# Kernel optimization log

Hardware: AMD Instinct MI355X
Metric: run time of the kernel (lower is better)

The kernel has to match this reference:

```python
import jax, jax.numpy as jnp
import numpy as np

B, S, D, H = 2, 2048, 1024, 16
HD = D // H  # 64
SCALE = np.sqrt(HD).astype(np.float32)


def setup_inputs() -> dict:
    key = jax.random.key(0)
    k1, k2, k3, k4, k5, k6 = jax.random.split(key, 6)
    hidden_states = jax.random.normal(k1, (B, S, D), dtype=jnp.float32)
    attention_mask = jax.random.randint(k2, (B, 1, S, S), 0, 2) > 0  # bool
    std = 0.02
    W_qkv = jax.random.normal(k3, (D, 3 * D), dtype=jnp.float32) * std
    b_qkv = jnp.zeros((3 * D,), dtype=jnp.float32)
    W_dense = jax.random.normal(k4, (D, D), dtype=jnp.float32) * std
    b_dense = jnp.zeros((D,), dtype=jnp.float32)
    return {
        "hidden_states": hidden_states,
        "attention_mask": attention_mask,
        "W_qkv": W_qkv,
        "b_qkv": b_qkv,
        "W_dense": W_dense,
        "b_dense": b_dense,
    }


def reference(hidden_states, attention_mask, W_qkv, b_qkv, W_dense, b_dense):
    # fused QKV projection: [B,S,3D]
    qkv = hidden_states @ W_qkv + b_qkv
    q, k, v = jnp.split(qkv, 3, axis=-1)
    # split heads -> [B,H,S,hd]
    q = q.reshape(B, S, H, HD).transpose(0, 2, 1, 3)
    k = k.reshape(B, S, H, HD).transpose(0, 2, 1, 3)
    v = v.reshape(B, S, H, HD).transpose(0, 2, 1, 3)
    # scores [B,H,S,S]
    scores = jnp.einsum("bhqd,bhkd->bhqk", q, k) / SCALE
    scores = jnp.where(attention_mask, scores, jnp.float32(-50000.0))
    probs = jax.nn.softmax(scores, axis=-1)
    ctx = jnp.einsum("bhqk,bhkd->bhqd", probs, v)
    # merge heads -> [B,S,D]
    ctx = ctx.transpose(0, 2, 1, 3).reshape(B, S, D)
    return ctx @ W_dense + b_dense
```

## Files before the change

kernel.cpp:

```cpp
#include <hip/hip_runtime.h>
#include <stdint.h>

#define B_ 2
#define S_ 2048
#define D_ 1024
#define H_ 16
#define HD_ 64
#define D3_ 3072
#define KD_ 1024

typedef __attribute__((ext_vector_type(8))) __bf16 bf16x8;
typedef __attribute__((ext_vector_type(4))) float f32x4;
typedef __attribute__((ext_vector_type(16))) float f32x16;
typedef __attribute__((ext_vector_type(4))) unsigned int u32x4;

typedef const __attribute__((address_space(1))) unsigned int gu32_t;
typedef __attribute__((address_space(3))) unsigned int lu32_t;

static __device__ __forceinline__ unsigned short f2bf(float f) {
  unsigned int u = __float_as_uint(f);
  u += 0x7fffu + ((u >> 16) & 1u);
  return (unsigned short)(u >> 16);
}

static __device__ __forceinline__ void gll16(const unsigned short* g, unsigned short* l) {
  __builtin_amdgcn_global_load_lds((gu32_t*)(const void*)g, (lu32_t*)(void*)l, 16, 0, 0);
}

static __device__ __forceinline__ bf16x8 lds_read8(const unsigned short* p) {
  return *reinterpret_cast<const bf16x8*>(p);
}

static __device__ __forceinline__ unsigned int cvtpk(float lo, float hi) {
  unsigned int r;
  asm("v_cvt_pk_bf16_f32 %0, %1, %2" : "=v"(r) : "v"(lo), "v"(hi));
  return r;
}

static __device__ __forceinline__ void plswap(unsigned int& a, unsigned int& b) {
  asm("v_permlane32_swap_b32 %0, %1" : "+v"(a), "+v"(b));
}

__global__ void cvt_bf16_kernel(const float* __restrict__ in, unsigned short* __restrict__ out, int n) {
  int i = (blockIdx.x * 256 + threadIdx.x) * 4;
  if (i >= n) return;
  float4 v = *reinterpret_cast<const float4*>(in + i);
  unsigned long long p = (unsigned long long)f2bf(v.x)
                       | ((unsigned long long)f2bf(v.y) << 16)
                       | ((unsigned long long)f2bf(v.z) << 32)
                       | ((unsigned long long)f2bf(v.w) << 48);
  *reinterpret_cast<unsigned long long*>(out + i) = p;
}

__global__ void tcvt_kernel(const float* __restrict__ in, unsigned short* __restrict__ out, int K, int N) {
  __shared__ float t[32][33];
  int k0 = blockIdx.y * 32, n0 = blockIdx.x * 32;
  int tx = threadIdx.x, ty = threadIdx.y;
  #pragma unroll
  for (int j = 0; j < 32; j += 8) t[ty + j][tx] = in[(size_t)(k0 + ty + j) * N + n0 + tx];
  __syncthreads();
  #pragma unroll
  for (int j = 0; j < 32; j += 8) out[(size_t)(n0 + ty + j) * K + k0 + tx] = f2bf(t[tx][ty + j]);
}

__global__ void mask_detect_kernel(const unsigned int* __restrict__ mw, unsigned int* __restrict__ flags) {
  __shared__ unsigned int red[2];
  if (threadIdx.x < 2) red[threadIdx.x] = 0;
  __syncthreads();
  unsigned int hb = 0, fl = 0;
  for (int i = threadIdx.x; i < 4096; i += 256) {
    unsigned int v = mw[i];
    hb |= (v & 0xFFFFFF00u);
    fl |= (v == 0x3F800000u) ? 1u : 0u;
  }
  atomicOr(&red[0], hb);
  atomicOr(&red[1], fl);
  __syncthreads();
  if (threadIdx.x == 0) flags[0] = red[1] ? 2u : (red[0] ? 1u : 0u);
}

__global__ void maskbits_kernel(const void* __restrict__ mask, const unsigned int* __restrict__ flags,
                                unsigned long long* __restrict__ bits) {
  const unsigned int mode = flags[0];
  const int lane = threadIdx.x & 63;
  const int nwaves = gridDim.x * 4;
  const int wid = (blockIdx.x * 256 + threadIdx.x) >> 6;
  const int total = (B_ * S_ * S_) / 256;
  for (int wb = wid; wb < total; wb += nwaves) {
    const size_t base = (size_t)wb * 256 + lane;
    unsigned long long m0, m1, m2, m3;
    if (mode == 0) {
      const int* p = (const int*)mask;
      m0 = __ballot(p[base] != 0);       m1 = __ballot(p[base + 64] != 0);
      m2 = __ballot(p[base + 128] != 0); m3 = __ballot(p[base + 192] != 0);
    } else if (mode == 1) {
      const unsigned char* p = (const unsigned char*)mask;
      m0 = __ballot(p[base] != 0);       m1 = __ballot(p[base + 64] != 0);
      m2 = __ballot(p[base + 128] != 0); m3 = __ballot(p[base + 192] != 0);
    } else {
      const float* p = (const float*)mask;
      m0 = __ballot(p[base] != 0.f);       m1 = __ballot(p[base + 64] != 0.f);
      m2 = __ballot(p[base + 128] != 0.f); m3 = __ballot(p[base + 192] != 0.f);
    }
    if (lane < 4) {
      unsigned long long v = (lane & 1) ? m1 : m0;
      unsigned long long w2 = (lane & 1) ? m3 : m2;
      v = (lane & 2) ? w2 : v;
      bits[(size_t)wb * 4 + lane] = v;
    }
  }
}

#define DSA256(BUF, MH, KC) \
  _Pragma("unroll") for (int fm_ = 0; fm_ < 4; ++fm_) \
    aq[fm_] = lds_read8(&Al[BUF][(wm * 128 + (MH) * 64 + fm_ * 16 + c16) * 64 + (KC)]);
#define DSB256(BUF, KC) \
  _Pragma("unroll") for (int fn_ = 0; fn_ < 4; ++fn_) \
    bq[fn_] = lds_read8(&Bl[BUF][(wn * 64 + fn_ * 16 + c16) * 64 + (KC)]);
#define MM256(MH) \
  __builtin_amdgcn_s_setprio(1); \
  _Pragma("unroll") for (int fm_ = 0; fm_ < 4; ++fm_) \
    _Pragma("unroll") for (int fn_ = 0; fn_ < 4; ++fn_) \
      acc[MH][fm_][fn_] = __builtin_amdgcn_mfma_f32_16x16x32_bf16(aq[fm_], bq[fn_], acc[MH][fm_][fn_], 0, 0, 0); \
  __builtin_amdgcn_s_setprio(0);
#define STA256(BUF, KT1) \
  _Pragma("unroll") for (int q_ = 0; q_ < 4; ++q_) \
    gll16(Ag + (size_t)(q_ * 64) * KD_ + (size_t)(KT1) * 64, &Al[BUF][q_ * 4096 + t * 8]);
#define STB256(BUF, KT1) \
  _Pragma("unroll") for (int q_ = 0; q_ < 4; ++q_) \
    gll16(Bg + (size_t)(q_ * 64) * KD_ + (size_t)(KT1) * 64, &Bl[BUF][q_ * 4096 + t * 8]);

__global__ __launch_bounds__(512, 2) void gemm256_kernel(
    const unsigned short* __restrict__ A,
    const unsigned short* __restrict__ Bt,
    const float* __restrict__ bias,
    unsigned short* __restrict__ Qh,
    unsigned short* __restrict__ Kh,
    unsigned short* __restrict__ Vt) {
  __shared__ unsigned short Al[2][16384];
  __shared__ unsigned short Bl[2][16384];
  const int t = threadIdx.x;
  const int lane = t & 63, w = t >> 6;
  const int g = lane >> 4, c16 = lane & 15;
  const int wm = w >> 2, wn = w & 3;

  const int wg = blockIdx.x;
  const int sw = (wg & 7) * 24 + (wg >> 3);
  const int by = sw / 12, bx = sw % 12;
  const int m0 = by * 256, n0 = bx * 256;

  f32x4 acc[2][4][4];
  #pragma unroll
  for (int mh = 0; mh < 2; ++mh)
    #pragma unroll
    for (int fm = 0; fm < 4; ++fm)
      #pragma unroll
      for (int fn = 0; fn < 4; ++fn)
        #pragma unroll
        for (int r = 0; r < 4; ++r) acc[mh][fm][fn][r] = 0.f;

  const int srow = t >> 3;
  const int scb = (t & 7) ^ (srow & 7);
  const unsigned short* Ag = A + (size_t)(m0 + srow) * KD_ + scb * 8;
  const unsigned short* Bg = Bt + (size_t)(n0 + srow) * KD_ + scb * 8;

  const int kc0 = ((g ^ (c16 & 7)) * 8);
  const int kc1 = (((4 + g) ^ (c16 & 7)) * 8);

  bf16x8 aq[4], bq[4];

  STA256(0, 0); STB256(0, 0);
  __syncthreads();

  #pragma unroll 1
  for (int kt = 0; kt < 16; ++kt) {
    const int buf = kt & 1, nb = buf ^ 1;
    const bool st = kt < 15;
    DSA256(buf, 0, kc0); DSB256(buf, kc0);
    if (st) STA256(nb, kt + 1);
    MM256(0);
    DSA256(buf, 1, kc0);
    if (st) STB256(nb, kt + 1);
    MM256(1);
    DSA256(buf, 0, kc1); DSB256(buf, kc1);
    MM256(0);
    DSA256(buf, 1, kc1);
    MM256(1);
    __syncthreads();
  }

  #pragma unroll
  for (int mh = 0; mh < 2; ++mh) {
    #pragma unroll
    for (int fn = 0; fn < 4; ++fn) {
      const int n = n0 + wn * 64 + fn * 16 + c16;
      const float bv = bias[n];
      const int sel = n >> 10;
      const int hh = (n & 1023) >> 6;
      const int d = n & 63;
      #pragma unroll
      for (int fm = 0; fm < 4; ++fm) {
        const int m_b = m0 + wm * 128 + mh * 64 + fm * 16 + g * 4;
        const int b = m_b >> 11;
        const int s0 = m_b & 2047;
        const int bh = b * H_ + hh;
        if (sel == 2) {
          ushort4 pk;
          pk.x = f2bf(acc[mh][fm][fn][0] + bv);
          pk.y = f2bf(acc[mh][fm][fn][1] + bv);
          pk.z = f2bf(acc[mh][fm][fn][2] + bv);
          pk.w = f2bf(acc[mh][fm][fn][3] + bv);
          *reinterpret_cast<ushort4*>(&Vt[(size_t)(bh * HD_ + d) * S_ + s0]) = pk;
        } else {
          #pragma unroll
          for (int r = 0; r < 4; ++r) {
            const float v = acc[mh][fm][fn][r] + bv;
            if (sel == 0) Qh[(size_t)(bh * S_ + s0 + r) * HD_ + d] = f2bf(v * 0.18033688011112042f);
            else          Kh[(size_t)(bh * S_ + s0 + r) * HD_ + d] = f2bf(v);
          }
        }
      }
    }
  }
}

__global__ void gemm_kernel(const unsigned short* __restrict__ A,
                            const unsigned short* __restrict__ Bt,
                            const float* __restrict__ bias,
                            int Ndim, int Kdim,
                            float* __restrict__ Out) {
  __shared__ unsigned short Asm[128 * 64];
  __shared__ unsigned short Bsm[128 * 64];
  const int t = threadIdx.x;
  const int lane = t & 63, w = t >> 6;
  const int g = lane >> 4, c16 = lane & 15;
  const int wr = w >> 1, wc = w & 1;
  const int m0 = blockIdx.y * 128, n0 = blockIdx.x * 128;

  f32x4 acc[4][4];
  #pragma unroll
  for (int mi = 0; mi < 4; ++mi)
    #pragma unroll
    for (int ni = 0; ni < 4; ++ni)
      #pragma unroll
      for (int r = 0; r < 4; ++r) acc[mi][ni][r] = 0.f;

  const int srow = t >> 3, scb = t & 7;
  const unsigned short* Ag = A + (size_t)(m0 + srow) * Kdim + scb * 8;
  const unsigned short* Bg = Bt + (size_t)(n0 + srow) * Kdim + scb * 8;
  unsigned short* ldsA = &Asm[w * 512];
  unsigned short* ldsB = &Bsm[w * 512];

  for (int kt = 0; kt < Kdim; kt += 64) {
    #pragma unroll
    for (int c = 0; c < 4; ++c) {
      gll16(Ag + (size_t)(c * 32) * Kdim + kt, ldsA + c * 2048);
      gll16(Bg + (size_t)(c * 32) * Kdim + kt, ldsB + c * 2048);
    }
    __syncthreads();
    #pragma unroll
    for (int ks = 0; ks < 2; ++ks) {
      bf16x8 af[4], bfr[4];
      #pragma unroll
      for (int i = 0; i < 4; ++i) {
        af[i]  = lds_read8(&Asm[(wr * 64 + i * 16 + c16) * 64 + ks * 32 + g * 8]);
        bfr[i] = lds_read8(&Bsm[(wc * 64 + i * 16 + c16) * 64 + ks * 32 + g * 8]);
      }
      #pragma unroll
      for (int mi = 0; mi < 4; ++mi)
        #pragma unroll
        for (int ni = 0; ni < 4; ++ni)
          acc[mi][ni] = __builtin_amdgcn_mfma_f32_16x16x32_bf16(af[mi], bfr[ni], acc[mi][ni], 0, 0, 0);
    }
    __syncthreads();
  }

  #pragma unroll
  for (int ni = 0; ni < 4; ++ni) {
    const int n = n0 + wc * 64 + ni * 16 + c16;
    const float bv = bias[n];
    #pragma unroll
    for (int mi = 0; mi < 4; ++mi) {
      #pragma unroll
      for (int r = 0; r < 4; ++r) {
        const int m = m0 + wr * 64 + mi * 16 + g * 4 + r;
        Out[(size_t)m * Ndim + n] = acc[mi][ni][r] + bv;
      }
    }
  }
}

#define PPOS(r) ((((r) & 3)) + 8 * ((r) >> 2))

#define SOFTPACK(SV, WQ, FLO, FHI) do {                                         \
    float p_[16];                                                               \
    _Pragma("unroll") for (int r_ = 0; r_ < 16; ++r_) {                         \
      float e_ = __builtin_amdgcn_exp2f((SV)[r_]);                              \
      int m_;                                                                   \
      asm("v_bfe_i32 %0, %1, %2, 1" : "=v"(m_) : "v"(WQ), "i"(PPOS(r_)));       \
      p_[r_] = __uint_as_float(__float_as_uint(e_) & (unsigned int)m_);         \
    }                                                                           \
    {                                                                           \
      unsigned int a0 = cvtpk(p_[0], p_[1]),  a1 = cvtpk(p_[2], p_[3]);         \
      unsigned int b0 = cvtpk(p_[4], p_[5]),  b1 = cvtpk(p_[6], p_[7]);         \
      plswap(a0, b0); plswap(a1, b1);                                           \
      u32x4 t_; t_[0] = a0; t_[1] = a1; t_[2] = b0; t_[3] = b1;                 \
      FLO = __builtin_bit_cast(bf16x8, t_);                                     \
    }                                                                           \
    {                                                                           \
      unsigned int a0 = cvtpk(p_[8], p_[9]),   a1 = cvtpk(p_[10], p_[11]);      \
      unsigned int b0 = cvtpk(p_[12], p_[13]), b1 = cvtpk(p_[14], p_[15]);      \
      plswap(a0, b0); plswap(a1, b1);                                           \
      u32x4 t_; t_[0] = a0; t_[1] = a1; t_[2] = b0; t_[3] = b1;                 \
      FHI = __builtin_bit_cast(bf16x8, t_);                                     \
    }                                                                           \
  } while (0)

#define PROC_KT(BUF, KT, WQW) do {                                              \
    f32x16 s0_;                                                                 \
    {                                                                           \
      bf16x8 kf_ = lds_read8(&sm[vp[0] + (BUF) * 8192 + (KT) * 2048]);          \
      s0_ = __builtin_amdgcn_mfma_f32_32x32x16_bf16(kf_, qf[0], zacc, 0, 0, 0); \
    }                                                                           \
    _Pragma("unroll") for (int kc_ = 1; kc_ < 4; ++kc_) {                       \
      bf16x8 kf_ = lds_read8(&sm[vp[kc_] + (BUF) * 8192 + (KT) * 2048]);        \
      s0_ = __builtin_amdgcn_mfma_f32_32x32x16_bf16(kf_, qf[kc_], s0_, 0, 0, 0); \
    }                                                                           \
    unsigned int wq_ = (WQW) >> sh4;                                            \
    bf16x8 paL_, paH_;                                                          \
    SOFTPACK(s0_, wq_, paL_, paH_);                                             \
    rsum = __builtin_amdgcn_mfma_f32_32x32x16_bf16(paL_, ones, rsum, 0, 0, 0);  \
    rsum = __builtin_amdgcn_mfma_f32_32x32x16_bf16(paH_, ones, rsum, 0, 0, 0);  \
    {                                                                           \
      bf16x8 vf0_ = lds_read8(&sm[vp[(KT)*2 + 0] + (BUF) * 8192 + 4096]);       \
      bf16x8 vf1_ = lds_read8(&sm[vp[(KT)*2 + 0] + (BUF) * 8192 + 4096 + 2048]); \
      ctx0 = __builtin_amdgcn_mfma_f32_32x32x16_bf16(paL_, vf0_, ctx0, 0, 0, 0); \
      ctx1 = __builtin_amdgcn_mfma_f32_32x32x16_bf16(paL_, vf1_, ctx1, 0, 0, 0); \
    }                                                                           \
    {                                                                           \
      bf16x8 vf0_ = lds_read8(&sm[vp[(KT)*2 + 1] + (BUF) * 8192 + 4096]);       \
      bf16x8 vf1_ = lds_read8(&sm[vp[(KT)*2 + 1] + (BUF) * 8192 + 4096 + 2048]); \
      ctx0 = __builtin_amdgcn_mfma_f32_32x32x16_bf16(paH_, vf0_, ctx0, 0, 0, 0); \
      ctx1 = __builtin_amdgcn_mfma_f32_32x32x16_bf16(paH_, vf1_, ctx1, 0, 0, 0); \
    }                                                                           \
  } while (0)

#define STAGE_TO(DBUF) do {                                                     \
    gll16(Kg,         &sm[kvb + (DBUF) * 8192 + qc1024]);                       \
    gll16(Kg + 512,   &sm[kvb + (DBUF) * 8192 + qc1024 + 512]);                 \
    gll16(Vg,         &sm[kvb + (DBUF) * 8192 + 4096 + qc1024]);                \
    gll16(Vg + 16384, &sm[kvb + (DBUF) * 8192 + 4096 + qc1024 + 512]);          \
    Kg += 4096; Vg += 64;                                                       \
  } while (0)

#define TILE64(BUF, KB, DOSTAGE) do {                                           \
    const uint2 mw_ = *(const uint2*)(mp + 2 * (KB));                           \
    if (DOSTAGE) STAGE_TO((BUF) ^ 1);                                           \
    PROC_KT(BUF, 0, mw_.x);                                                     \
    PROC_KT(BUF, 1, mw_.y);                                                     \
    __syncthreads();                                                            \
  } while (0)

__global__ __launch_bounds__(512, 4) void flash_kernel(
    const unsigned short* __restrict__ Qh,
    const unsigned short* __restrict__ Kh,
    const unsigned short* __restrict__ Vt,
    const unsigned long long* __restrict__ mbits,
    unsigned short* __restrict__ Ctx) {
  __shared__ unsigned short sm[32768];
  const int t = threadIdx.x;
  const int lane = t & 63, w = t >> 6;
  const int hi = lane >> 5, l31 = lane & 31;
  const int grp = w >> 2, qc = w & 3;
  const int h = blockIdx.y, b = blockIdx.z;
  const int bh = b * H_ + h;
  const int qrow = blockIdx.x * 128 + qc * 32 + l31;
  const int sh4 = hi * 4;
  const int kvb = grp * 16384;
  const int qc1024 = qc * 1024;

  bf16x8 qf[4];
  {
    const unsigned short* Qr = Qh + (size_t)(bh * S_ + qrow) * HD_ + hi * 8;
    #pragma unroll
    for (int kc = 0; kc < 4; ++kc) qf[kc] = *reinterpret_cast<const bf16x8*>(Qr + kc * 16);
  }

  f32x16 ctx0, ctx1, rsum, zacc;
  #pragma unroll
  for (int i = 0; i < 16; ++i) { ctx0[i] = 0.f; ctx1[i] = 0.f; rsum[i] = 0.f; zacc[i] = 0.f; }
  bf16x8 ones;
  #pragma unroll
  for (int i = 0; i < 8; ++i) ones[i] = (__bf16)1.0f;

  int vp[4];
  #pragma unroll
  for (int c = 0; c < 4; ++c)
    vp[c] = grp * 16384 + l31 * 64 + (((2 * c + hi) ^ (l31 & 7)) * 8);

  const unsigned int* mp =
      (const unsigned int*)(mbits + (size_t)(b * S_ + qrow) * 32) + grp * 32;

  const int srw = lane >> 3;
  const int scb = (lane & 7) ^ (srw & 7);
  const unsigned short* Kg = Kh + (size_t)(bh * S_ + grp * 1024 + qc * 16 + srw) * HD_ + scb * 8;
  const unsigned short* Vg = Vt + (size_t)(bh * HD_ + qc * 16 + srw) * S_ + grp * 1024 + scb * 8;

  STAGE_TO(0);
  __syncthreads();

  #pragma unroll 1
  for (int kb = 0; kb < 16; kb += 2) {
    TILE64(0, kb, 1);
    TILE64(1, kb + 1, (kb < 14));
  }

  float* creg = (float*)sm;
  if (grp == 1) {
    float* ex = creg + qc * 3072 + lane;
    #pragma unroll
    for (int r = 0; r < 16; ++r) {
      ex[r * 64] = ctx0[r];
      ex[(16 + r) * 64] = ctx1[r];
      ex[(32 + r) * 64] = rsum[r];
    }
  }
  __syncthreads();
  if (grp == 0) {
    const float* im = creg + qc * 3072 + lane;
    #pragma unroll
    for (int r = 0; r < 16; ++r) {
      const float c0 = ctx0[r] + im[r * 64];
      const float c1 = ctx1[r] + im[(16 + r) * 64];
      const float rt = rsum[r] + im[(32 + r) * 64];
      const float iv = 1.0f / rt;
      const int sq = blockIdx.x * 128 + qc * 32 + PPOS(r) + 4 * hi;
      unsigned short* op = Ctx + (size_t)(b * S_ + sq) * D_ + h * HD_ + l31;
      op[0]  = f2bf(c0 * iv);
      op[32] = f2bf(c1 * iv);
    }
  }
}

extern "C" void kernel_launch(void* const* d_in, const int* in_sizes, int n_in,
                              void* d_out, int out_size, void* d_ws, size_t ws_size,
                              hipStream_t stream) {
  const float* hidden  = (const float*)d_in[0];
  const void*  mask    = d_in[1];
  const float* W_qkv   = (const float*)d_in[2];
  const float* b_qkv   = (const float*)d_in[3];
  const float* W_dense = (const float*)d_in[4];
  const float* b_dense = (const float*)d_in[5];
  float* out = (float*)d_out;

  char* ws = (char*)d_ws;
  unsigned short* Qh   = (unsigned short*)(ws);
  unsigned short* Kh   = (unsigned short*)(ws + 8388608);
  unsigned short* Vtb  = (unsigned short*)(ws + 16777216);
  unsigned short* Xb   = (unsigned short*)(ws + 25165824);
  unsigned short* Ctx  = Xb;
  unsigned short* Wqt  = (unsigned short*)(ws + 33554432);
  unsigned short* Wdt  = Wqt;
  unsigned long long* mbits = (unsigned long long*)(ws + 39845888);
  unsigned int* flags  = (unsigned int*)(ws + 40894464);

  cvt_bf16_kernel<<<4096, 256, 0, stream>>>(hidden, Xb, B_ * S_ * D_);
  tcvt_kernel<<<dim3(D3_ / 32, D_ / 32), dim3(32, 8), 0, stream>>>(W_qkv, Wqt, D_, D3_);
  mask_detect_kernel<<<1, 256, 0, stream>>>((const unsigned int*)mask, flags);
  maskbits_kernel<<<1024, 256, 0, stream>>>(mask, flags, mbits);

  gemm256_kernel<<<192, 512, 0, stream>>>(Xb, Wqt, b_qkv, Qh, Kh, Vtb);

  tcvt_kernel<<<dim3(D_ / 32, D_ / 32), dim3(32, 8), 0, stream>>>(W_dense, Wdt, D_, D_);

  flash_kernel<<<dim3(S_ / 128, H_, B_), 512, 0, stream>>>(Qh, Kh, Vtb, mbits, Ctx);

  gemm_kernel<<<dim3(D_ / 128, (B_ * S_) / 128), 256, 0, stream>>>(
      Ctx, Wdt, b_dense, D_, D_, out);
}
```

Before: 143.2 us.

## Fuse preprocessing kernels and double-buffer the output projection GEMM

Three prep launches (hidden-state bf16 conversion, W_qkv transpose, mask bitpacking) are merged into one prep_kernel with block-range dispatch, cutting launch overhead and serialization. The output-projection GEMM is replaced by a double-buffered, XOR-swizzled LDS version that prefetches the next K tile during MFMAs, plus a block-index swizzle for L2 locality. The mask-detect kernel still runs first, and the prep kernel's mask section depends on its flags. LDS use doubles, which may limit occupancy.

New measurement: 130.2 us. 1.1x faster.

```diff
diff --git a/kernel.cpp b/kernel.cpp
--- a/kernel.cpp
+++ b/kernel.cpp
@@ -41,28 +41,6 @@
   asm("v_permlane32_swap_b32 %0, %1" : "+v"(a), "+v"(b));
 }
 
-__global__ void cvt_bf16_kernel(const float* __restrict__ in, unsigned short* __restrict__ out, int n) {
-  int i = (blockIdx.x * 256 + threadIdx.x) * 4;
-  if (i >= n) return;
-  float4 v = *reinterpret_cast<const float4*>(in + i);
-  unsigned long long p = (unsigned long long)f2bf(v.x)
-                       | ((unsigned long long)f2bf(v.y) << 16)
-                       | ((unsigned long long)f2bf(v.z) << 32)
-                       | ((unsigned long long)f2bf(v.w) << 48);
-  *reinterpret_cast<unsigned long long*>(out + i) = p;
-}
-
-__global__ void tcvt_kernel(const float* __restrict__ in, unsigned short* __restrict__ out, int K, int N) {
-  __shared__ float t[32][33];
-  int k0 = blockIdx.y * 32, n0 = blockIdx.x * 32;
-  int tx = threadIdx.x, ty = threadIdx.y;
-  #pragma unroll
-  for (int j = 0; j < 32; j += 8) t[ty + j][tx] = in[(size_t)(k0 + ty + j) * N + n0 + tx];
-  __syncthreads();
-  #pragma unroll
-  for (int j = 0; j < 32; j += 8) out[(size_t)(n0 + ty + j) * K + k0 + tx] = f2bf(t[tx][ty + j]);
-}
-
 __global__ void mask_detect_kernel(const unsigned int* __restrict__ mw, unsigned int* __restrict__ flags) {
   __shared__ unsigned int red[2];
   if (threadIdx.x < 2) red[threadIdx.x] = 0;
@@ -79,36 +57,72 @@
   if (threadIdx.x == 0) flags[0] = red[1] ? 2u : (red[0] ? 1u : 0u);
 }
 
-__global__ void maskbits_kernel(const void* __restrict__ mask, const unsigned int* __restrict__ flags,
-                                unsigned long long* __restrict__ bits) {
-  const unsigned int mode = flags[0];
-  const int lane = threadIdx.x & 63;
-  const int nwaves = gridDim.x * 4;
-  const int wid = (blockIdx.x * 256 + threadIdx.x) >> 6;
-  const int total = (B_ * S_ * S_) / 256;
-  for (int wb = wid; wb < total; wb += nwaves) {
-    const size_t base = (size_t)wb * 256 + lane;
-    unsigned long long m0, m1, m2, m3;
-    if (mode == 0) {
-      const int* p = (const int*)mask;
-      m0 = __ballot(p[base] != 0);       m1 = __ballot(p[base + 64] != 0);
-      m2 = __ballot(p[base + 128] != 0); m3 = __ballot(p[base + 192] != 0);
-    } else if (mode == 1) {
-      const unsigned char* p = (const unsigned char*)mask;
-      m0 = __ballot(p[base] != 0);       m1 = __ballot(p[base + 64] != 0);
-      m2 = __ballot(p[base + 128] != 0); m3 = __ballot(p[base + 192] != 0);
-    } else {
-      const float* p = (const float*)mask;
-      m0 = __ballot(p[base] != 0.f);       m1 = __ballot(p[base + 64] != 0.f);
-      m2 = __ballot(p[base + 128] != 0.f); m3 = __ballot(p[base + 192] != 0.f);
+static __device__ __forceinline__ void transpose32(const float* __restrict__ in,
+                                                   unsigned short* __restrict__ out,
+                                                   int K, int N, int bx, int by, int t,
+                                                   float (*tsm)[33]) {
+  const int k0 = by * 32, n0 = bx * 32;
+  const int tx = t & 31, ty = t >> 5;
+  #pragma unroll
+  for (int j = 0; j < 32; j += 8) tsm[ty + j][tx] = in[(size_t)(k0 + ty + j) * N + n0 + tx];
+  __syncthreads();
+  #pragma unroll
+  for (int j = 0; j < 32; j += 8) out[(size_t)(n0 + ty + j) * K + k0 + tx] = f2bf(tsm[tx][ty + j]);
+}
+
+__global__ void prep_kernel(const float* __restrict__ hidden, unsigned short* __restrict__ Xb,
+                            const float* __restrict__ Wq, unsigned short* __restrict__ Wqt,
+                            const void* __restrict__ mask, const unsigned int* __restrict__ flags,
+                            unsigned long long* __restrict__ bits) {
+  __shared__ float tsm[32][33];
+  const int bid = blockIdx.x;
+  const int t = threadIdx.x;
+  if (bid < 4096) {
+    const int i = (bid * 256 + t) * 4;
+    float4 v = *reinterpret_cast<const float4*>(hidden + i);
+    unsigned long long p = (unsigned long long)f2bf(v.x)
+                         | ((unsigned long long)f2bf(v.y) << 16)
+                         | ((unsigned long long)f2bf(v.z) << 32)
+                         | ((unsigned long long)f2bf(v.w) << 48);
+    *reinterpret_cast<unsigned long long*>(Xb + i) = p;
+  } else if (bid < 7168) {
+    const int bb = bid - 4096;
+    transpose32(Wq, Wqt, KD_, D3_, bb % 96, bb / 96, t, tsm);
+  } else {
+    const unsigned int mode = flags[0];
+    const int lane = t & 63;
+    const int nwaves = 1024 * 4;
+    const int wid = ((bid - 7168) * 256 + t) >> 6;
+    const int total = (B_ * S_ * S_) / 256;
+    for (int wb = wid; wb < total; wb += nwaves) {
+      const size_t base = (size_t)wb * 256 + lane;
+      unsigned long long m0, m1, m2, m3;
+      if (mode == 0) {
+        const int* p = (const int*)mask;
+        m0 = __ballot(p[base] != 0);       m1 = __ballot(p[base + 64] != 0);
+        m2 = __ballot(p[base + 128] != 0); m3 = __ballot(p[base + 192] != 0);
+      } else if (mode == 1) {
+        const unsigned char* p = (const unsigned char*)mask;
+        m0 = __ballot(p[base] != 0);       m1 = __ballot(p[base + 64] != 0);
+        m2 = __ballot(p[base + 128] != 0); m3 = __ballot(p[base + 192] != 0);
+      } else {
+        const float* p = (const float*)mask;
+        m0 = __ballot(p[base] != 0.f);       m1 = __ballot(p[base + 64] != 0.f);
+        m2 = __ballot(p[base + 128] != 0.f); m3 = __ballot(p[base + 192] != 0.f);
+      }
+      if (lane < 4) {
+        unsigned long long v = (lane & 1) ? m1 : m0;
+        unsigned long long w2 = (lane & 1) ? m3 : m2;
+        v = (lane & 2) ? w2 : v;
+        bits[(size_t)wb * 4 + lane] = v;
+      }
     }
-    if (lane < 4) {
-      unsigned long long v = (lane & 1) ? m1 : m0;
-      unsigned long long w2 = (lane & 1) ? m3 : m2;
-      v = (lane & 2) ? w2 : v;
-      bits[(size_t)wb * 4 + lane] = v;
-    }
-  }
+  }
+}
+
+__global__ void tcvt_kernel(const float* __restrict__ in, unsigned short* __restrict__ out, int K, int N) {
+  __shared__ float tsm[32][33];
+  transpose32(in, out, K, N, blockIdx.x, blockIdx.y, threadIdx.x, tsm);
 }
 
 #define DSA256(BUF, MH, KC) \
@@ -224,18 +238,42 @@
   }
 }
 
-__global__ void gemm_kernel(const unsigned short* __restrict__ A,
-                            const unsigned short* __restrict__ Bt,
-                            const float* __restrict__ bias,
-                            int Ndim, int Kdim,
-                            float* __restrict__ Out) {
-  __shared__ unsigned short Asm[128 * 64];
-  __shared__ unsigned short Bsm[128 * 64];
+#define DDA(BUF, KC) \
+  _Pragma("unroll") for (int i_ = 0; i_ < 4; ++i_) \
+    aq[i_] = lds_read8(&Al[BUF][(wr * 64 + i_ * 16 + c16) * 64 + (KC)]);
+#define DDB(BUF, KC) \
+  _Pragma("unroll") for (int i_ = 0; i_ < 4; ++i_) \
+    bq[i_] = lds_read8(&Bl[BUF][(wc * 64 + i_ * 16 + c16) * 64 + (KC)]);
+#define DMM \
+  __builtin_amdgcn_s_setprio(1); \
+  _Pragma("unroll") for (int mi_ = 0; mi_ < 4; ++mi_) \
+    _Pragma("unroll") for (int ni_ = 0; ni_ < 4; ++ni_) \
+      acc[mi_][ni_] = __builtin_amdgcn_mfma_f32_16x16x32_bf16(aq[mi_], bq[ni_], acc[mi_][ni_], 0, 0, 0); \
+  __builtin_amdgcn_s_setprio(0);
+#define DSTA(BUF, KT1) \
+  _Pragma("unroll") for (int q_ = 0; q_ < 4; ++q_) \
+    gll16(Ag + (size_t)(q_ * 32) * KD_ + (size_t)(KT1) * 64, &Al[BUF][q_ * 2048 + t * 8]);
+#define DSTB(BUF, KT1) \
+  _Pragma("unroll") for (int q_ = 0; q_ < 4; ++q_) \
+    gll16(Bg + (size_t)(q_ * 32) * KD_ + (size_t)(KT1) * 64, &Bl[BUF][q_ * 2048 + t * 8]);
+
+__global__ __launch_bounds__(256, 2) void gemm128p_kernel(
+    const unsigned short* __restrict__ A,
+    const unsigned short* __restrict__ Bt,
+    const float* __restrict__ bias,
+    int Ndim,
+    float* __restrict__ Out) {
+  __shared__ unsigned short Al[2][8192];
+  __shared__ unsigned short Bl[2][8192];
   const int t = threadIdx.x;
   const int lane = t & 63, w = t >> 6;
   const int g = lane >> 4, c16 = lane & 15;
   const int wr = w >> 1, wc = w & 1;
-  const int m0 = blockIdx.y * 128, n0 = blockIdx.x * 128;
+
+  const int wg = blockIdx.x;
+  const int sw = (wg & 7) * 32 + (wg >> 3);
+  const int by = sw >> 3, bx = sw & 7;
+  const int m0 = by * 128, n0 = bx * 128;
 
   f32x4 acc[4][4];
   #pragma unroll
@@ -245,33 +283,29 @@
       #pragma unroll
       for (int r = 0; r < 4; ++r) acc[mi][ni][r] = 0.f;
 
-  const int srow = t >> 3, scb = t & 7;
-  const unsigned short* Ag = A + (size_t)(m0 + srow) * Kdim + scb * 8;
-  const unsigned short* Bg = Bt + (size_t)(n0 + srow) * Kdim + scb * 8;
-  unsigned short* ldsA = &Asm[w * 512];
-  unsigned short* ldsB = &Bsm[w * 512];
-
-  for (int kt = 0; kt < Kdim; kt += 64) {
-    #pragma unroll
-    for (int c = 0; c < 4; ++c) {
-      gll16(Ag + (size_t)(c * 32) * Kdim + kt, ldsA + c * 2048);
-      gll16(Bg + (size_t)(c * 32) * Kdim + kt, ldsB + c * 2048);
-    }
-    __syncthreads();
-    #pragma unroll
-    for (int ks = 0; ks < 2; ++ks) {
-      bf16x8 af[4], bfr[4];
-      #pragma unroll
-      for (int i = 0; i < 4; ++i) {
-        af[i]  = lds_read8(&Asm[(wr * 64 + i * 16 + c16) * 64 + ks * 32 + g * 8]);
-        bfr[i] = lds_read8(&Bsm[(wc * 64 + i * 16 + c16) * 64 + ks * 32 + g * 8]);
-      }
-      #pragma unroll
-      for (int mi = 0; mi < 4; ++mi)
-        #pragma unroll
-        for (int ni = 0; ni < 4; ++ni)
-          acc[mi][ni] = __builtin_amdgcn_mfma_f32_16x16x32_bf16(af[mi], bfr[ni], acc[mi][ni], 0, 0, 0);
-    }
+  const int srow = t >> 3;
+  const int scb = (t & 7) ^ (srow & 7);
+  const unsigned short* Ag = A + (size_t)(m0 + srow) * KD_ + scb * 8;
+  const unsigned short* Bg = Bt + (size_t)(n0 + srow) * KD_ + scb * 8;
+
+  const int kc0 = ((g ^ (c16 & 7)) * 8);
+  const int kc1 = (((4 + g) ^ (c16 & 7)) * 8);
+
+  bf16x8 aq[4], bq[4];
+
+  DSTA(0, 0); DSTB(0, 0);
+  __syncthreads();
+
+  #pragma unroll 1
+  for (int kt = 0; kt < 16; ++kt) {
+    const int buf = kt & 1, nb = buf ^ 1;
+    const bool st = kt < 15;
+    DDA(buf, kc0); DDB(buf, kc0);
+    if (st) DSTA(nb, kt + 1);
+    DMM;
+    DDA(buf, kc1); DDB(buf, kc1);
+    if (st) DSTB(nb, kt + 1);
+    DMM;
     __syncthreads();
   }
 
@@ -464,17 +498,14 @@
   unsigned long long* mbits = (unsigned long long*)(ws + 39845888);
   unsigned int* flags  = (unsigned int*)(ws + 40894464);
 
-  cvt_bf16_kernel<<<4096, 256, 0, stream>>>(hidden, Xb, B_ * S_ * D_);
-  tcvt_kernel<<<dim3(D3_ / 32, D_ / 32), dim3(32, 8), 0, stream>>>(W_qkv, Wqt, D_, D3_);
   mask_detect_kernel<<<1, 256, 0, stream>>>((const unsigned int*)mask, flags);
-  maskbits_kernel<<<1024, 256, 0, stream>>>(mask, flags, mbits);
+  prep_kernel<<<8192, 256, 0, stream>>>(hidden, Xb, W_qkv, Wqt, mask, flags, mbits);
 
   gemm256_kernel<<<192, 512, 0, stream>>>(Xb, Wqt, b_qkv, Qh, Kh, Vtb);
 
-  tcvt_kernel<<<dim3(D_ / 32, D_ / 32), dim3(32, 8), 0, stream>>>(W_dense, Wdt, D_, D_);
+  tcvt_kernel<<<dim3(D_ / 32, D_ / 32), 256, 0, stream>>>(W_dense, Wdt, D_, D_);
 
   flash_kernel<<<dim3(S_ / 128, H_, B_), 512, 0, stream>>>(Qh, Kh, Vtb, mbits, Ctx);
 
-  gemm_kernel<<<dim3(D_ / 128, (B_ * S_) / 128), 256, 0, stream>>>(
-      Ctx, Wdt, b_dense, D_, D_, out);
-}
+  gemm128p_kernel<<<256, 256, 0, stream>>>(Ctx, Wdt, b_dense, D_, out);
+}
```
